# Kernel tuning notes

Hardware: AMD Instinct MI355X
Metric: run time of the kernel (lower is better)

Reference implementation:

```python
import jax, jax.numpy as jnp
import numpy as np
import math

D = 1024
H = 16
C = D // H
EPS = 1e-5

def layernorm(x, g, b):
    mu = jnp.mean(x, axis=-1, keepdims=True)
    var = jnp.mean(jnp.square(x - mu), axis=-1, keepdims=True)
    return (x - mu) * jax.lax.rsqrt(var + EPS) * g + b

def setup_inputs() -> dict:
    key = jax.random.key(0)
    ks = jax.random.split(key, 12)
    s = 1.0 / math.sqrt(D)
    inp = {
        "x": jax.random.normal(ks[0], (4, 2048, D), dtype=jnp.float32),
        "src_mask": jnp.ones((4, 2048), dtype=bool),
        "Wk": jax.random.normal(ks[1], (D, D), dtype=jnp.float32) * s,
        "Wq": jax.random.normal(ks[2], (D, D), dtype=jnp.float32) * s,
        "Wv": jax.random.normal(ks[3], (D, D), dtype=jnp.float32) * s,
        "Wfc": jax.random.normal(ks[4], (D, D), dtype=jnp.float32) * s,
        "bfc": jnp.zeros((D,), dtype=jnp.float32),
        "g1": jnp.ones((D,), dtype=jnp.float32),
        "b1": jnp.zeros((D,), dtype=jnp.float32),
        "g2": jnp.ones((D,), dtype=jnp.float32),
        "b2": jnp.zeros((D,), dtype=jnp.float32),
        "W1": jax.random.normal(ks[5], (D, 4 * D), dtype=jnp.float32) * s,
        "bf1": jnp.zeros((4 * D,), dtype=jnp.float32),
        "W2": jax.random.normal(ks[6], (4 * D, D), dtype=jnp.float32) * (1.0 / math.sqrt(4 * D)),
        "bf2": jnp.zeros((D,), dtype=jnp.float32),
    }
    return inp

def reference(x, src_mask, Wk, Wq, Wv, Wfc, bfc, g1, b1, g2, b2, W1, bf1, W2, bf2):
    b, s, _ = x.shape
    xl = layernorm(x, g1, b1)
    # self-attention (src_mask is unused in the original module)
    k = (xl @ Wk).reshape(b, s, H, C).transpose(0, 2, 1, 3)  # bhsc
    q = (xl @ Wq).reshape(b, s, H, C).transpose(0, 2, 1, 3)
    v = (xl @ Wv).reshape(b, s, H, C).transpose(0, 2, 1, 3)
    # NOTE: original multiplies by sqrt(c) (not divide) -- faithful quirk
    scores = jnp.einsum('bhqc,bhkc->bhqk', q, k) * math.sqrt(C)
    attn = jax.nn.softmax(scores, axis=-1)
    o = jnp.einsum('bhqk,bhkc->bhqc', attn, v)
    o = o.transpose(0, 2, 1, 3).reshape(b, s, D)
    ka = o @ Wfc + bfc
    x = ka + x
    xl2 = layernorm(x, g2, b2)
    ff = jax.nn.relu(xl2 @ W1 + bf1) @ W2 + bf2
    return ff + x
```

## Files before the change

### kernel.cpp

```cpp
#include <hip/hip_runtime.h>
#include <hip/hip_bf16.h>
#include <math.h>


typedef __hip_bfloat16 bf16_t;
typedef __bf16 bf16x8 __attribute__((ext_vector_type(8)));
typedef float f32x4 __attribute__((ext_vector_type(4)));

#define LN_EPS 1e-5f
#define QSCALE 11.541560327111707f
#define RESCALE_THR 100.0f
#define M0_PRIOR 275.0f

__device__ __forceinline__ void async_copy16(const bf16_t* g, bf16_t* l) {
  __builtin_amdgcn_global_load_lds(
      (const __attribute__((address_space(1))) void*)g,
      (__attribute__((address_space(3))) void*)l,
      16 , 0 , 0 );
}

__device__ __forceinline__ void split_bf16(float v, bf16_t& hi, bf16_t& lo) {
  hi = __float2bfloat16(v);
  lo = __float2bfloat16(v - __bfloat162float(hi));
}

template<bool SPLIT>
__global__ __launch_bounds__(256) void ln_kernel(
    const float* __restrict__ x, const float* __restrict__ g,
    const float* __restrict__ b, bf16_t* __restrict__ out_hi,
    bf16_t* __restrict__ out_lo)
{
  const int row = blockIdx.x;
  const int tid = threadIdx.x;
  const float4 v = *(const float4*)(x + (size_t)row * 1024 + tid * 4);
  float s  = v.x + v.y + v.z + v.w;
  float ss = v.x * v.x + v.y * v.y + v.z * v.z + v.w * v.w;
  for (int off = 32; off > 0; off >>= 1) {
    s  += __shfl_down(s, off);
    ss += __shfl_down(ss, off);
  }
  __shared__ float sb[4], ssb[4];
  const int wave = tid >> 6, lane = tid & 63;
  if (lane == 0) { sb[wave] = s; ssb[wave] = ss; }
  __syncthreads();
  const float tot  = sb[0] + sb[1] + sb[2] + sb[3];
  const float tots = ssb[0] + ssb[1] + ssb[2] + ssb[3];
  const float mu   = tot * (1.0f / 1024.0f);
  const float var  = tots * (1.0f / 1024.0f) - mu * mu;
  const float rstd = rsqrtf(var + LN_EPS);
  const float4 gv = *(const float4*)(g + tid * 4);
  const float4 bv = *(const float4*)(b + tid * 4);
  float y[4] = {(v.x - mu) * rstd * gv.x + bv.x,
                (v.y - mu) * rstd * gv.y + bv.y,
                (v.z - mu) * rstd * gv.z + bv.z,
                (v.w - mu) * rstd * gv.w + bv.w};
  bf16_t hi[4] __attribute__((aligned(8)));
  bf16_t lo[4] __attribute__((aligned(8)));
  #pragma unroll
  for (int i = 0; i < 4; i++) split_bf16(y[i], hi[i], lo[i]);
  uint2 ph, pl;
  __builtin_memcpy(&ph, hi, 8);
  *(uint2*)(out_hi + (size_t)row * 1024 + tid * 4) = ph;
  if (SPLIT) {
    __builtin_memcpy(&pl, lo, 8);
    *(uint2*)(out_lo + (size_t)row * 1024 + tid * 4) = pl;
  }
}

__global__ __launch_bounds__(256) void wtrans_all_kernel(
    const float* __restrict__ Wq, const float* __restrict__ Wk,
    const float* __restrict__ Wv, const float* __restrict__ Wfc,
    const float* __restrict__ W1, const float* __restrict__ W2,
    bf16_t* __restrict__ WqkH, bf16_t* __restrict__ WqkL,
    bf16_t* __restrict__ WvT, bf16_t* __restrict__ WfcT,
    bf16_t* __restrict__ W1T, bf16_t* __restrict__ W2T)
{
  const int id = blockIdx.x;
  const float* W; bf16_t* DH; bf16_t* DL = nullptr;
  int K, N, n0, k0;
  if (id < 4096) {
    K = 1024; N = 1024;
    const int local = id & 1023;
    n0 = (local & 31) * 32; k0 = (local >> 5) * 32;
    if (id < 1024)      { W = Wq;  DH = WqkH;                 DL = WqkL; }
    else if (id < 2048) { W = Wk;  DH = WqkH + 1024 * 1024;   DL = WqkL + 1024 * 1024; }
    else if (id < 3072) { W = Wv;  DH = WvT; }
    else                { W = Wfc; DH = WfcT; }
  } else if (id < 8192) {
    const int local = id - 4096;
    K = 1024; N = 4096; W = W1; DH = W1T;
    n0 = (local & 127) * 32; k0 = (local >> 7) * 32;
  } else {
    const int local = id - 8192;
    K = 4096; N = 1024; W = W2; DH = W2T;
    n0 = (local & 31) * 32; k0 = (local >> 5) * 32;
  }
  __shared__ float t[32][33];
  const int tx = threadIdx.x & 31, ty = threadIdx.x >> 5;
  #pragma unroll
  for (int r = ty; r < 32; r += 8)
    t[r][tx] = W[(size_t)(k0 + r) * N + n0 + tx];
  __syncthreads();
  #pragma unroll
  for (int r = ty; r < 32; r += 8) {
    const float v = t[tx][r];
    bf16_t hi, lo;
    split_bf16(v, hi, lo);
    DH[(size_t)(n0 + r) * K + k0 + tx] = hi;
    if (DL) DL[(size_t)(n0 + r) * K + k0 + tx] = lo;
  }
}

template<bool BIAS, bool RELU, bool RESID, bool OUTBF>
__global__ __launch_bounds__(256) void gemm_kernel(
    const bf16_t* __restrict__ A, const bf16_t* __restrict__ BT,
    const float* __restrict__ bias, const float* __restrict__ resid,
    float* __restrict__ outF, bf16_t* __restrict__ outB,
    int M, int N, int K)
{
  __shared__ __align__(16) bf16_t As[128 * 64];
  __shared__ __align__(16) bf16_t Bs[128 * 64];
  const int nblk = N >> 7;
  const int bm = blockIdx.x / nblk;
  const int bn = blockIdx.x % nblk;
  const int tid  = threadIdx.x;
  const int wave = tid >> 6;
  const int lane = tid & 63;
  const int l15  = lane & 15;
  const int quad = lane >> 4;
  const int wm = wave >> 1, wn = wave & 1;

  const int srow = lane >> 3;
  const int schunk = (lane & 7) ^ srow;
  const bf16_t* aG = A  + (size_t)(bm * 128 + wave * 32 + srow) * K + schunk * 8;
  const bf16_t* bG = BT + (size_t)(bn * 128 + wave * 32 + srow) * K + schunk * 8;

  f32x4 acc[4][4];
  #pragma unroll
  for (int i = 0; i < 4; i++)
    #pragma unroll
    for (int j = 0; j < 4; j++) acc[i][j] = (f32x4){0.f, 0.f, 0.f, 0.f};

  const int rsw = l15 & 7;

  for (int kt = 0; kt < K; kt += 64) {
    #pragma unroll
    for (int j = 0; j < 4; j++) {
      async_copy16(aG + kt + (size_t)(j * 8) * K, &As[(wave * 32 + j * 8) * 64]);
      async_copy16(bG + kt + (size_t)(j * 8) * K, &Bs[(wave * 32 + j * 8) * 64]);
    }
    __syncthreads();
    #pragma unroll
    for (int ko = 0; ko < 2; ko++) {
      bf16x8 af[4], bfr[4];
      #pragma unroll
      for (int i = 0; i < 4; i++)
        af[i]  = *(const bf16x8*)&As[(wm * 64 + i * 16 + l15) * 64 +
                                     (((ko * 4 + quad) ^ rsw) * 8)];
      #pragma unroll
      for (int j = 0; j < 4; j++)
        bfr[j] = *(const bf16x8*)&Bs[(wn * 64 + j * 16 + l15) * 64 +
                                     (((ko * 4 + quad) ^ rsw) * 8)];
      #pragma unroll
      for (int i = 0; i < 4; i++)
        #pragma unroll
        for (int j = 0; j < 4; j++)
          acc[i][j] = __builtin_amdgcn_mfma_f32_16x16x32_bf16(af[i], bfr[j], acc[i][j], 0, 0, 0);
    }
    __syncthreads();
  }

  const int gm0 = bm * 128 + wm * 64 + quad * 4;
  const int gn0 = bn * 128 + wn * 64 + l15;
  #pragma unroll
  for (int i = 0; i < 4; i++) {
    #pragma unroll
    for (int j = 0; j < 4; j++) {
      const int gn = gn0 + j * 16;
      const float bz = BIAS ? bias[gn] : 0.0f;
      #pragma unroll
      for (int r = 0; r < 4; r++) {
        const int gm = gm0 + i * 16 + r;
        float v = acc[i][j][r] + bz;
        if (RESID) v += resid[(size_t)gm * N + gn];
        if (RELU)  v = fmaxf(v, 0.0f);
        if (OUTBF) outB[(size_t)gm * N + gn] = __float2bfloat16(v);
        else       outF[(size_t)gm * N + gn] = v;
      }
    }
  }
}

__global__ __launch_bounds__(256) void gemm_split_kernel(
    const bf16_t* __restrict__ Ah, const bf16_t* __restrict__ Al,
    const bf16_t* __restrict__ Bh, const bf16_t* __restrict__ Bl,
    bf16_t* __restrict__ out_hi, bf16_t* __restrict__ out_lo,
    int M, int N, int K)
{
  __shared__ __align__(16) bf16_t AsH[128 * 32];
  __shared__ __align__(16) bf16_t AsL[128 * 32];
  __shared__ __align__(16) bf16_t BsH[128 * 32];
  __shared__ __align__(16) bf16_t BsL[128 * 32];
  const int nblk = N >> 7;
  const int bm = blockIdx.x / nblk;
  const int bn = blockIdx.x % nblk;
  const int tid  = threadIdx.x;
  const int wave = tid >> 6;
  const int lane = tid & 63;
  const int l15  = lane & 15;
  const int quad = lane >> 4;
  const int wm = wave >> 1, wn = wave & 1;

  const int srow = lane >> 2;
  const int schunk = (lane & 3) ^ ((lane >> 3) & 3);
  const size_t aOff = (size_t)(bm * 128 + wave * 32 + srow) * K + schunk * 8;
  const size_t bOff = (size_t)(bn * 128 + wave * 32 + srow) * K + schunk * 8;
  const int ldsOff0 = (wave * 32) * 32;
  const int ldsOff1 = (wave * 32 + 16) * 32;

  f32x4 acc[4][4];
  #pragma unroll
  for (int i = 0; i < 4; i++)
    #pragma unroll
    for (int j = 0; j < 4; j++) acc[i][j] = (f32x4){0.f, 0.f, 0.f, 0.f};

  const int rsw = (l15 >> 1) & 3;

  for (int kt = 0; kt < K; kt += 32) {
    async_copy16(Ah + aOff + kt, &AsH[ldsOff0]);
    async_copy16(Ah + aOff + kt + (size_t)16 * K, &AsH[ldsOff1]);
    async_copy16(Al + aOff + kt, &AsL[ldsOff0]);
    async_copy16(Al + aOff + kt + (size_t)16 * K, &AsL[ldsOff1]);
    async_copy16(Bh + bOff + kt, &BsH[ldsOff0]);
    async_copy16(Bh + bOff + kt + (size_t)16 * K, &BsH[ldsOff1]);
    async_copy16(Bl + bOff + kt, &BsL[ldsOff0]);
    async_copy16(Bl + bOff + kt + (size_t)16 * K, &BsL[ldsOff1]);
    __syncthreads();
    bf16x8 afH[4], afL[4], bfH[4], bfL[4];
    #pragma unroll
    for (int i = 0; i < 4; i++) {
      const int o = (wm * 64 + i * 16 + l15) * 32 + ((quad ^ rsw) * 8);
      afH[i] = *(const bf16x8*)&AsH[o];
      afL[i] = *(const bf16x8*)&AsL[o];
    }
    #pragma unroll
    for (int j = 0; j < 4; j++) {
      const int o = (wn * 64 + j * 16 + l15) * 32 + ((quad ^ rsw) * 8);
      bfH[j] = *(const bf16x8*)&BsH[o];
      bfL[j] = *(const bf16x8*)&BsL[o];
    }
    #pragma unroll
    for (int i = 0; i < 4; i++)
      #pragma unroll
      for (int j = 0; j < 4; j++) {
        acc[i][j] = __builtin_amdgcn_mfma_f32_16x16x32_bf16(afH[i], bfH[j], acc[i][j], 0, 0, 0);
        acc[i][j] = __builtin_amdgcn_mfma_f32_16x16x32_bf16(afH[i], bfL[j], acc[i][j], 0, 0, 0);
        acc[i][j] = __builtin_amdgcn_mfma_f32_16x16x32_bf16(afL[i], bfH[j], acc[i][j], 0, 0, 0);
      }
    __syncthreads();
  }

  const int gm0 = bm * 128 + wm * 64 + quad * 4;
  const int gn0 = bn * 128 + wn * 64 + l15;
  #pragma unroll
  for (int i = 0; i < 4; i++)
    #pragma unroll
    for (int j = 0; j < 4; j++) {
      const int gn = gn0 + j * 16;
      const float scale = (gn < 1024) ? QSCALE : 1.0f;
      #pragma unroll
      for (int r = 0; r < 4; r++) {
        const int gm = gm0 + i * 16 + r;
        bf16_t hi, lo;
        split_bf16(acc[i][j][r] * scale, hi, lo);
        out_hi[(size_t)gm * N + gn] = hi;
        out_lo[(size_t)gm * N + gn] = lo;
      }
    }
}

__global__ __launch_bounds__(256) void attn_kernel(
    const bf16_t* __restrict__ qkH,
    const bf16_t* __restrict__ qkL,
    const bf16_t* __restrict__ vT,
    bf16_t* __restrict__ o)
{
  const int lin   = blockIdx.x;
  const int slice = (lin & 7) * 8 + ((lin >> 3) & 7);
  const int qt    = lin >> 6;
  const int h     = slice & 15;
  const int b     = slice >> 4;
  const int wave = threadIdx.x >> 6;
  const int lane = threadIdx.x & 63;
  const int l15  = lane & 15;
  const int quad = lane >> 4;
  const int sw   = l15 & 7;
  const int qrowA = qt * 128 + wave * 32;
  const int qrowB = qrowA + 16;

  __shared__ __align__(16) bf16_t SMEM[20480];
  bf16_t* pw = SMEM + 16384 + wave * 1024;

  const size_t tok0 = (size_t)b * 2048;
  const size_t qoffA = (tok0 + qrowA + l15) * 2048 + h * 64;
  const size_t qoffB = (tok0 + qrowB + l15) * 2048 + h * 64;
  const bf16x8 aA0H = *(const bf16x8*)(qkH + qoffA + quad * 8);
  const bf16x8 aA1H = *(const bf16x8*)(qkH + qoffA + 32 + quad * 8);
  const bf16x8 aA0L = *(const bf16x8*)(qkL + qoffA + quad * 8);
  const bf16x8 aA1L = *(const bf16x8*)(qkL + qoffA + 32 + quad * 8);
  const bf16x8 aB0H = *(const bf16x8*)(qkH + qoffB + quad * 8);
  const bf16x8 aB1H = *(const bf16x8*)(qkH + qoffB + 32 + quad * 8);
  const bf16x8 aB0L = *(const bf16x8*)(qkL + qoffB + quad * 8);
  const bf16x8 aB1L = *(const bf16x8*)(qkL + qoffB + 32 + quad * 8);

  const int kOff = 1024 + h * 64;
  const int rsub = lane >> 3;
  const int csw  = (lane & 7) ^ rsub;

  const bf16_t* vRow[4];
  #pragma unroll
  for (int c = 0; c < 4; c++)
    vRow[c] = vT + (size_t)(h * 64 + c * 16 + l15) * 8192 + tok0 + quad * 8;

  f32x4 negMA = (f32x4){-M0_PRIOR, -M0_PRIOR, -M0_PRIOR, -M0_PRIOR};
  f32x4 negMB = negMA;
  f32x4 OfA[4], OfB[4];
  f32x4 lsumA = (f32x4){0.f, 0.f, 0.f, 0.f};
  f32x4 lsumB = lsumA;
  #pragma unroll
  for (int c = 0; c < 4; c++) { OfA[c] = lsumA; OfB[c] = lsumA; }

  #pragma unroll
  for (int j = 0; j < 2; j++) {
    const int row0 = wave * 16 + j * 8;
    const size_t krow = tok0 + row0 + rsub;
    async_copy16(qkH + krow * 2048 + kOff + csw * 8, &SMEM[row0 * 64]);
    async_copy16(qkL + krow * 2048 + kOff + csw * 8, &SMEM[8192 + row0 * 64]);
  }
  __syncthreads();

  for (int i = 0; i < 32; i++) {
    const int kbase = i * 64;
    const int co = (i & 1) * 4096;
    const int no = 4096 - co;
    if (i < 31) {
      #pragma unroll
      for (int j = 0; j < 2; j++) {
        const int row0 = wave * 16 + j * 8;
        const size_t krow = tok0 + kbase + 64 + row0 + rsub;
        async_copy16(qkH + krow * 2048 + kOff + csw * 8, &SMEM[no + row0 * 64]);
        async_copy16(qkL + krow * 2048 + kOff + csw * 8, &SMEM[8192 + no + row0 * 64]);
      }
    }
    const bf16_t* KhC = SMEM + co;
    const bf16_t* KlC = SMEM + 8192 + co;

    #pragma unroll
    for (int half = 0; half < 2; half++) {
      const int koff = kbase + half * 32;
      bf16x8 bv[4];
      #pragma unroll
      for (int c = 0; c < 4; c++)
        bv[c] = *(const bf16x8*)(vRow[c] + koff);

      #pragma unroll
      for (int tl = 0; tl < 2; tl++) {
        const int t = half * 2 + tl;
        const int base = (t * 16 + l15) * 64;
        const bf16x8 bh0 = *(const bf16x8*)&KhC[base + ((quad) ^ sw) * 8];
        const bf16x8 bh1 = *(const bf16x8*)&KhC[base + ((4 + quad) ^ sw) * 8];
        const bf16x8 bl0 = *(const bf16x8*)&KlC[base + ((quad) ^ sw) * 8];
        const bf16x8 bl1 = *(const bf16x8*)&KlC[base + ((4 + quad) ^ sw) * 8];
        f32x4 accA = negMA;
        f32x4 accB = negMB;
        __builtin_amdgcn_s_setprio(1);
        accA = __builtin_amdgcn_mfma_f32_16x16x32_bf16(aA0H, bh0, accA, 0, 0, 0);
        accA = __builtin_amdgcn_mfma_f32_16x16x32_bf16(aA1H, bh1, accA, 0, 0, 0);
        accA = __builtin_amdgcn_mfma_f32_16x16x32_bf16(aA0H, bl0, accA, 0, 0, 0);
        accA = __builtin_amdgcn_mfma_f32_16x16x32_bf16(aA1H, bl1, accA, 0, 0, 0);
        accA = __builtin_amdgcn_mfma_f32_16x16x32_bf16(aA0L, bh0, accA, 0, 0, 0);
        accA = __builtin_amdgcn_mfma_f32_16x16x32_bf16(aA1L, bh1, accA, 0, 0, 0);
        accB = __builtin_amdgcn_mfma_f32_16x16x32_bf16(aB0H, bh0, accB, 0, 0, 0);
        accB = __builtin_amdgcn_mfma_f32_16x16x32_bf16(aB1H, bh1, accB, 0, 0, 0);
        accB = __builtin_amdgcn_mfma_f32_16x16x32_bf16(aB0H, bl0, accB, 0, 0, 0);
        accB = __builtin_amdgcn_mfma_f32_16x16x32_bf16(aB1H, bl1, accB, 0, 0, 0);
        accB = __builtin_amdgcn_mfma_f32_16x16x32_bf16(aB0L, bh0, accB, 0, 0, 0);
        accB = __builtin_amdgcn_mfma_f32_16x16x32_bf16(aB1L, bh1, accB, 0, 0, 0);
        __builtin_amdgcn_s_setprio(0);

        float pmax = fmaxf(fmaxf(fmaxf(accA[0], accA[1]), fmaxf(accA[2], accA[3])),
                           fmaxf(fmaxf(accB[0], accB[1]), fmaxf(accB[2], accB[3])));
        if (!__all(pmax <= RESCALE_THR)) {
          #pragma unroll
          for (int r = 0; r < 4; r++) {
            float mA = accA[r], mB = accB[r];
            mA = fmaxf(mA, __shfl_xor(mA, 1)); mB = fmaxf(mB, __shfl_xor(mB, 1));
            mA = fmaxf(mA, __shfl_xor(mA, 2)); mB = fmaxf(mB, __shfl_xor(mB, 2));
            mA = fmaxf(mA, __shfl_xor(mA, 4)); mB = fmaxf(mB, __shfl_xor(mB, 4));
            mA = fmaxf(mA, __shfl_xor(mA, 8)); mB = fmaxf(mB, __shfl_xor(mB, 8));
            const float sA = fmaxf(mA, 0.0f);
            const float sB = fmaxf(mB, 0.0f);
            const float fA = __builtin_amdgcn_exp2f(-sA);
            const float fB = __builtin_amdgcn_exp2f(-sB);
            negMA[r] -= sA;  negMB[r] -= sB;
            lsumA[r] *= fA;  lsumB[r] *= fB;
            #pragma unroll
            for (int c = 0; c < 4; c++) { OfA[c][r] *= fA; OfB[c][r] *= fB; }
            accA[r] -= sA;   accB[r] -= sB;
            if (tl == 1) {
              const int RA = quad * 4 + r;
              const int RB = 16 + RA;
              const int ksw = (RA >> 1) & 3;
              const int iA = RA * 32 + (((l15 >> 3) ^ ksw) * 8) + (l15 & 7);
              const int iB = RB * 32 + (((l15 >> 3) ^ ksw) * 8) + (l15 & 7);
              pw[iA] = __float2bfloat16(__bfloat162float(pw[iA]) * fA);
              pw[iB] = __float2bfloat16(__bfloat162float(pw[iB]) * fB);
            }
          }
        }

        #pragma unroll
        for (int r = 0; r < 4; r++) {
          const float pA = __builtin_amdgcn_exp2f(accA[r]);
          const float pB = __builtin_amdgcn_exp2f(accB[r]);
          lsumA[r] += pA;
          lsumB[r] += pB;
          const int RA = quad * 4 + r;
          const int RB = 16 + RA;
          const int chunk = tl * 2 + (l15 >> 3);
          const int ksw = (RA >> 1) & 3;
          pw[RA * 32 + ((chunk ^ ksw) * 8) + (l15 & 7)] = __float2bfloat16(pA);
          pw[RB * 32 + ((chunk ^ ksw) * 8) + (l15 & 7)] = __float2bfloat16(pB);
        }
      }

      const int psw = (l15 >> 1) & 3;
      const bf16x8 paA = *(const bf16x8*)&pw[l15 * 32 + ((quad ^ psw) * 8)];
      const bf16x8 paB = *(const bf16x8*)&pw[(16 + l15) * 32 + ((quad ^ psw) * 8)];
      __builtin_amdgcn_s_setprio(1);
      #pragma unroll
      for (int c = 0; c < 4; c++) {
        OfA[c] = __builtin_amdgcn_mfma_f32_16x16x32_bf16(paA, bv[c], OfA[c], 0, 0, 0);
        OfB[c] = __builtin_amdgcn_mfma_f32_16x16x32_bf16(paB, bv[c], OfB[c], 0, 0, 0);
      }
      __builtin_amdgcn_s_setprio(0);
    }
    __syncthreads();
  }

  float lrowA[4], lrowB[4];
  #pragma unroll
  for (int r = 0; r < 4; r++) {
    float cA = lsumA[r], cB = lsumB[r];
    cA += __shfl_xor(cA, 1); cB += __shfl_xor(cB, 1);
    cA += __shfl_xor(cA, 2); cB += __shfl_xor(cB, 2);
    cA += __shfl_xor(cA, 4); cB += __shfl_xor(cB, 4);
    cA += __shfl_xor(cA, 8); cB += __shfl_xor(cB, 8);
    lrowA[r] = cA; lrowB[r] = cB;
  }

  bf16_t* opA = o + (tok0 + qrowA) * 1024 + h * 64;
  bf16_t* opB = o + (tok0 + qrowB) * 1024 + h * 64;
  #pragma unroll
  for (int c = 0; c < 4; c++)
    #pragma unroll
    for (int r = 0; r < 4; r++) {
      opA[(size_t)(quad * 4 + r) * 1024 + c * 16 + l15] =
          __float2bfloat16(OfA[c][r] / lrowA[r]);
      opB[(size_t)(quad * 4 + r) * 1024 + c * 16 + l15] =
          __float2bfloat16(OfB[c][r] / lrowB[r]);
    }
}

extern "C" void kernel_launch(void* const* d_in, const int* in_sizes, int n_in,
                              void* d_out, int out_size, void* d_ws, size_t ws_size,
                              hipStream_t stream)
{
  (void)in_sizes; (void)n_in; (void)out_size; (void)ws_size;
  const float* x   = (const float*)d_in[0];
  const float* Wk  = (const float*)d_in[2];
  const float* Wq  = (const float*)d_in[3];
  const float* Wv  = (const float*)d_in[4];
  const float* Wfc = (const float*)d_in[5];
  const float* bfc = (const float*)d_in[6];
  const float* g1  = (const float*)d_in[7];
  const float* b1  = (const float*)d_in[8];
  const float* g2  = (const float*)d_in[9];
  const float* b2  = (const float*)d_in[10];
  const float* W1  = (const float*)d_in[11];
  const float* bf1 = (const float*)d_in[12];
  const float* W2  = (const float*)d_in[13];
  const float* bf2 = (const float*)d_in[14];
  float* out = (float*)d_out;

  char* ws = (char*)d_ws;
  bf16_t* xl_hi  = (bf16_t*)(ws + (0ull   << 20));
  bf16_t* oAtt   = xl_hi;
  bf16_t* xl_lo  = (bf16_t*)(ws + (16ull  << 20));
  bf16_t* vT     = xl_lo;
  bf16_t* xl2    = xl_lo;
  bf16_t* qk_hi  = (bf16_t*)(ws + (32ull  << 20));
  bf16_t* qk_lo  = (bf16_t*)(ws + (64ull  << 20));
  bf16_t* h1     = qk_hi;
  float*  x2     = (float*) (ws + (112ull << 20));
  bf16_t* Wqk_hi = (bf16_t*)(ws + (144ull << 20));
  bf16_t* Wqk_lo = (bf16_t*)(ws + (148ull << 20));
  bf16_t* WvT    = (bf16_t*)(ws + (152ull << 20));
  bf16_t* WfcT   = (bf16_t*)(ws + (154ull << 20));
  bf16_t* W1T    = (bf16_t*)(ws + (156ull << 20));
  bf16_t* W2T    = (bf16_t*)(ws + (164ull << 20));

  const dim3 blk(256);

  wtrans_all_kernel<<<12288, blk, 0, stream>>>(
      Wq, Wk, Wv, Wfc, W1, W2, Wqk_hi, Wqk_lo, WvT, WfcT, W1T, W2T);

  ln_kernel<true><<<8192, blk, 0, stream>>>(x, g1, b1, xl_hi, xl_lo);

  gemm_split_kernel<<<64 * 16, blk, 0, stream>>>(
      xl_hi, xl_lo, Wqk_hi, Wqk_lo, qk_hi, qk_lo, 8192, 2048, 1024);

  gemm_kernel<false, false, false, true><<<8 * 64, blk, 0, stream>>>(
      WvT, xl_hi, nullptr, nullptr, nullptr, vT, 1024, 8192, 1024);

  attn_kernel<<<dim3(1024), blk, 0, stream>>>(qk_hi, qk_lo, vT, oAtt);

  gemm_kernel<true, false, true, false><<<64 * 8, blk, 0, stream>>>(
      oAtt, WfcT, bfc, x, x2, nullptr, 8192, 1024, 1024);

  ln_kernel<false><<<8192, blk, 0, stream>>>(x2, g2, b2, xl2, nullptr);

  gemm_kernel<true, true, false, true><<<64 * 32, blk, 0, stream>>>(
      xl2, W1T, bf1, nullptr, nullptr, h1, 8192, 4096, 1024);

  gemm_kernel<true, false, true, false><<<64 * 8, blk, 0, stream>>>(
      h1, W2T, bf2, x2, out, nullptr, 8192, 1024, 4096);
}
```

Measured before the change: 709.9 us.

## Transpose QK^T MFMA so softmax rows map to lanes; swizzle GEMM block order

The attention kernel swaps the MFMA operands for S=QK^T, so each lane holds four keys of one query row. Row max and row sum now use two cross-quad shuffles per tile instead of four per element, and P is written to LDS as packed 32-bit bf16 pairs. The rescale path and the final normalization fetch per-row factors with a lane shuffle and multiply by a reciprocal instead of dividing. Both GEMM kernels also remap block indices in groups of eight, aiming for better L2 locality across XCDs, at the cost of more intricate index logic.

```diff
diff --git a/kernel.cpp b/kernel.cpp
--- a/kernel.cpp
+++ b/kernel.cpp
@@ -22,6 +22,14 @@
 __device__ __forceinline__ void split_bf16(float v, bf16_t& hi, bf16_t& lo) {
   hi = __float2bfloat16(v);
   lo = __float2bfloat16(v - __bfloat162float(hi));
+}
+
+__device__ __forceinline__ unsigned pack_bf16(float lo, float hi) {
+  bf16_t a = __float2bfloat16(lo), b = __float2bfloat16(hi);
+  unsigned short ua, ub;
+  __builtin_memcpy(&ua, &a, 2);
+  __builtin_memcpy(&ub, &b, 2);
+  return (unsigned)ua | ((unsigned)ub << 16);
 }
 
 template<bool SPLIT>
@@ -121,8 +129,9 @@
   __shared__ __align__(16) bf16_t As[128 * 64];
   __shared__ __align__(16) bf16_t Bs[128 * 64];
   const int nblk = N >> 7;
-  const int bm = blockIdx.x / nblk;
-  const int bn = blockIdx.x % nblk;
+  const int wg = (blockIdx.x & 7) * (gridDim.x >> 3) + (blockIdx.x >> 3);
+  const int bm = wg / nblk;
+  const int bn = wg % nblk;
   const int tid  = threadIdx.x;
   const int wave = tid >> 6;
   const int lane = tid & 63;
@@ -202,8 +211,9 @@
   __shared__ __align__(16) bf16_t BsH[128 * 32];
   __shared__ __align__(16) bf16_t BsL[128 * 32];
   const int nblk = N >> 7;
-  const int bm = blockIdx.x / nblk;
-  const int bn = blockIdx.x % nblk;
+  const int wg = (blockIdx.x & 7) * (gridDim.x >> 3) + (blockIdx.x >> 3);
+  const int bm = wg / nblk;
+  const int bn = wg % nblk;
   const int tid  = threadIdx.x;
   const int wave = tid >> 6;
   const int lane = tid & 63;
@@ -300,6 +310,7 @@
 
   __shared__ __align__(16) bf16_t SMEM[20480];
   bf16_t* pw = SMEM + 16384 + wave * 1024;
+  unsigned* pw32 = (unsigned*)pw;
 
   const size_t tok0 = (size_t)b * 2048;
   const size_t qoffA = (tok0 + qrowA + l15) * 2048 + h * 64;
@@ -322,13 +333,18 @@
   for (int c = 0; c < 4; c++)
     vRow[c] = vT + (size_t)(h * 64 + c * 16 + l15) * 8192 + tok0 + quad * 8;
 
-  f32x4 negMA = (f32x4){-M0_PRIOR, -M0_PRIOR, -M0_PRIOR, -M0_PRIOR};
-  f32x4 negMB = negMA;
+  const int psw = (l15 >> 1) & 3;
+  const int wbaseA = l15 * 16 + (quad & 1) * 2;
+  const int wbaseB = wbaseA + 256;
+
+  float negMA = -M0_PRIOR, negMB = -M0_PRIOR;
+  float lsumA = 0.f, lsumB = 0.f;
   f32x4 OfA[4], OfB[4];
-  f32x4 lsumA = (f32x4){0.f, 0.f, 0.f, 0.f};
-  f32x4 lsumB = lsumA;
-  #pragma unroll
-  for (int c = 0; c < 4; c++) { OfA[c] = lsumA; OfB[c] = lsumA; }
+  #pragma unroll
+  for (int c = 0; c < 4; c++) {
+    OfA[c] = (f32x4){0.f, 0.f, 0.f, 0.f};
+    OfB[c] = (f32x4){0.f, 0.f, 0.f, 0.f};
+  }
 
   #pragma unroll
   for (int j = 0; j < 2; j++) {
@@ -371,70 +387,88 @@
         const bf16x8 bh1 = *(const bf16x8*)&KhC[base + ((4 + quad) ^ sw) * 8];
         const bf16x8 bl0 = *(const bf16x8*)&KlC[base + ((quad) ^ sw) * 8];
         const bf16x8 bl1 = *(const bf16x8*)&KlC[base + ((4 + quad) ^ sw) * 8];
-        f32x4 accA = negMA;
-        f32x4 accB = negMB;
+        f32x4 accA = (f32x4){negMA, negMA, negMA, negMA};
+        f32x4 accB = (f32x4){negMB, negMB, negMB, negMB};
         __builtin_amdgcn_s_setprio(1);
-        accA = __builtin_amdgcn_mfma_f32_16x16x32_bf16(aA0H, bh0, accA, 0, 0, 0);
-        accA = __builtin_amdgcn_mfma_f32_16x16x32_bf16(aA1H, bh1, accA, 0, 0, 0);
-        accA = __builtin_amdgcn_mfma_f32_16x16x32_bf16(aA0H, bl0, accA, 0, 0, 0);
-        accA = __builtin_amdgcn_mfma_f32_16x16x32_bf16(aA1H, bl1, accA, 0, 0, 0);
-        accA = __builtin_amdgcn_mfma_f32_16x16x32_bf16(aA0L, bh0, accA, 0, 0, 0);
-        accA = __builtin_amdgcn_mfma_f32_16x16x32_bf16(aA1L, bh1, accA, 0, 0, 0);
-        accB = __builtin_amdgcn_mfma_f32_16x16x32_bf16(aB0H, bh0, accB, 0, 0, 0);
-        accB = __builtin_amdgcn_mfma_f32_16x16x32_bf16(aB1H, bh1, accB, 0, 0, 0);
-        accB = __builtin_amdgcn_mfma_f32_16x16x32_bf16(aB0H, bl0, accB, 0, 0, 0);
-        accB = __builtin_amdgcn_mfma_f32_16x16x32_bf16(aB1H, bl1, accB, 0, 0, 0);
-        accB = __builtin_amdgcn_mfma_f32_16x16x32_bf16(aB0L, bh0, accB, 0, 0, 0);
-        accB = __builtin_amdgcn_mfma_f32_16x16x32_bf16(aB1L, bh1, accB, 0, 0, 0);
+        accA = __builtin_amdgcn_mfma_f32_16x16x32_bf16(bh0, aA0H, accA, 0, 0, 0);
+        accA = __builtin_amdgcn_mfma_f32_16x16x32_bf16(bh1, aA1H, accA, 0, 0, 0);
+        accA = __builtin_amdgcn_mfma_f32_16x16x32_bf16(bl0, aA0H, accA, 0, 0, 0);
+        accA = __builtin_amdgcn_mfma_f32_16x16x32_bf16(bl1, aA1H, accA, 0, 0, 0);
+        accA = __builtin_amdgcn_mfma_f32_16x16x32_bf16(bh0, aA0L, accA, 0, 0, 0);
+        accA = __builtin_amdgcn_mfma_f32_16x16x32_bf16(bh1, aA1L, accA, 0, 0, 0);
+        accB = __builtin_amdgcn_mfma_f32_16x16x32_bf16(bh0, aB0H, accB, 0, 0, 0);
+        accB = __builtin_amdgcn_mfma_f32_16x16x32_bf16(bh1, aB1H, accB, 0, 0, 0);
+        accB = __builtin_amdgcn_mfma_f32_16x16x32_bf16(bl0, aB0H, accB, 0, 0, 0);
+        accB = __builtin_amdgcn_mfma_f32_16x16x32_bf16(bl1, aB1H, accB, 0, 0, 0);
+        accB = __builtin_amdgcn_mfma_f32_16x16x32_bf16(bh0, aB0L, accB, 0, 0, 0);
+        accB = __builtin_amdgcn_mfma_f32_16x16x32_bf16(bh1, aB1L, accB, 0, 0, 0);
         __builtin_amdgcn_s_setprio(0);
 
         float pmax = fmaxf(fmaxf(fmaxf(accA[0], accA[1]), fmaxf(accA[2], accA[3])),
                            fmaxf(fmaxf(accB[0], accB[1]), fmaxf(accB[2], accB[3])));
         if (!__all(pmax <= RESCALE_THR)) {
+          float mA = fmaxf(fmaxf(accA[0], accA[1]), fmaxf(accA[2], accA[3]));
+          float mB = fmaxf(fmaxf(accB[0], accB[1]), fmaxf(accB[2], accB[3]));
+          mA = fmaxf(mA, __shfl_xor(mA, 16)); mB = fmaxf(mB, __shfl_xor(mB, 16));
+          mA = fmaxf(mA, __shfl_xor(mA, 32)); mB = fmaxf(mB, __shfl_xor(mB, 32));
+          const float sA = fmaxf(mA, 0.0f);
+          const float sB = fmaxf(mB, 0.0f);
+          const float fA = __builtin_amdgcn_exp2f(-sA);
+          const float fB = __builtin_amdgcn_exp2f(-sB);
+          negMA -= sA;  negMB -= sB;
+          lsumA *= fA;  lsumB *= fB;
           #pragma unroll
           for (int r = 0; r < 4; r++) {
-            float mA = accA[r], mB = accB[r];
-            mA = fmaxf(mA, __shfl_xor(mA, 1)); mB = fmaxf(mB, __shfl_xor(mB, 1));
-            mA = fmaxf(mA, __shfl_xor(mA, 2)); mB = fmaxf(mB, __shfl_xor(mB, 2));
-            mA = fmaxf(mA, __shfl_xor(mA, 4)); mB = fmaxf(mB, __shfl_xor(mB, 4));
-            mA = fmaxf(mA, __shfl_xor(mA, 8)); mB = fmaxf(mB, __shfl_xor(mB, 8));
-            const float sA = fmaxf(mA, 0.0f);
-            const float sB = fmaxf(mB, 0.0f);
-            const float fA = __builtin_amdgcn_exp2f(-sA);
-            const float fB = __builtin_amdgcn_exp2f(-sB);
-            negMA[r] -= sA;  negMB[r] -= sB;
-            lsumA[r] *= fA;  lsumB[r] *= fB;
+            accA[r] -= sA;  accB[r] -= sB;
+          }
+          #pragma unroll
+          for (int r = 0; r < 4; r++) {
+            const int src = quad * 20 + r;
+            const float fqA = __shfl(fA, src);
+            const float fqB = __shfl(fB, src);
             #pragma unroll
-            for (int c = 0; c < 4; c++) { OfA[c][r] *= fA; OfB[c][r] *= fB; }
-            accA[r] -= sA;   accB[r] -= sB;
-            if (tl == 1) {
-              const int RA = quad * 4 + r;
-              const int RB = 16 + RA;
-              const int ksw = (RA >> 1) & 3;
-              const int iA = RA * 32 + (((l15 >> 3) ^ ksw) * 8) + (l15 & 7);
-              const int iB = RB * 32 + (((l15 >> 3) ^ ksw) * 8) + (l15 & 7);
-              pw[iA] = __float2bfloat16(__bfloat162float(pw[iA]) * fA);
-              pw[iB] = __float2bfloat16(__bfloat162float(pw[iB]) * fB);
+            for (int c = 0; c < 4; c++) { OfA[c][r] *= fqA; OfB[c][r] *= fqB; }
+          }
+          if (tl == 1) {
+            asm volatile("" ::: "memory");
+            const int slot0 = (quad >> 1) ^ psw;
+            const int iA = wbaseA + slot0 * 4;
+            const int iB = wbaseB + slot0 * 4;
+            #pragma unroll
+            for (int j2 = 0; j2 < 2; j2++) {
+              unsigned ua = pw32[iA + j2], ub = pw32[iB + j2];
+              float a0 = __uint_as_float((ua & 0xffffu) << 16) * fA;
+              float a1 = __uint_as_float(ua & 0xffff0000u) * fA;
+              float b0 = __uint_as_float((ub & 0xffffu) << 16) * fB;
+              float b1 = __uint_as_float(ub & 0xffff0000u) * fB;
+              pw32[iA + j2] = pack_bf16(a0, a1);
+              pw32[iB + j2] = pack_bf16(b0, b1);
             }
+            asm volatile("" ::: "memory");
           }
         }
 
-        #pragma unroll
-        for (int r = 0; r < 4; r++) {
-          const float pA = __builtin_amdgcn_exp2f(accA[r]);
-          const float pB = __builtin_amdgcn_exp2f(accB[r]);
-          lsumA[r] += pA;
-          lsumB[r] += pB;
-          const int RA = quad * 4 + r;
-          const int RB = 16 + RA;
-          const int chunk = tl * 2 + (l15 >> 3);
-          const int ksw = (RA >> 1) & 3;
-          pw[RA * 32 + ((chunk ^ ksw) * 8) + (l15 & 7)] = __float2bfloat16(pA);
-          pw[RB * 32 + ((chunk ^ ksw) * 8) + (l15 & 7)] = __float2bfloat16(pB);
-        }
+        const float pA0 = __builtin_amdgcn_exp2f(accA[0]);
+        const float pA1 = __builtin_amdgcn_exp2f(accA[1]);
+        const float pA2 = __builtin_amdgcn_exp2f(accA[2]);
+        const float pA3 = __builtin_amdgcn_exp2f(accA[3]);
+        const float pB0 = __builtin_amdgcn_exp2f(accB[0]);
+        const float pB1 = __builtin_amdgcn_exp2f(accB[1]);
+        const float pB2 = __builtin_amdgcn_exp2f(accB[2]);
+        const float pB3 = __builtin_amdgcn_exp2f(accB[3]);
+        lsumA += (pA0 + pA1) + (pA2 + pA3);
+        lsumB += (pB0 + pB1) + (pB2 + pB3);
+        const int slot = ((tl * 2) + (quad >> 1)) ^ psw;
+        const int iA = wbaseA + slot * 4;
+        const int iB = wbaseB + slot * 4;
+        pw32[iA]     = pack_bf16(pA0, pA1);
+        pw32[iA + 1] = pack_bf16(pA2, pA3);
+        pw32[iB]     = pack_bf16(pB0, pB1);
+        pw32[iB + 1] = pack_bf16(pB2, pB3);
       }
 
-      const int psw = (l15 >> 1) & 3;
+      asm volatile("" ::: "memory");
+
       const bf16x8 paA = *(const bf16x8*)&pw[l15 * 32 + ((quad ^ psw) * 8)];
       const bf16x8 paB = *(const bf16x8*)&pw[(16 + l15) * 32 + ((quad ^ psw) * 8)];
       __builtin_amdgcn_s_setprio(1);
@@ -444,32 +478,31 @@
         OfB[c] = __builtin_amdgcn_mfma_f32_16x16x32_bf16(paB, bv[c], OfB[c], 0, 0, 0);
       }
       __builtin_amdgcn_s_setprio(0);
+
+      asm volatile("" ::: "memory");
     }
     __syncthreads();
   }
 
-  float lrowA[4], lrowB[4];
-  #pragma unroll
-  for (int r = 0; r < 4; r++) {
-    float cA = lsumA[r], cB = lsumB[r];
-    cA += __shfl_xor(cA, 1); cB += __shfl_xor(cB, 1);
-    cA += __shfl_xor(cA, 2); cB += __shfl_xor(cB, 2);
-    cA += __shfl_xor(cA, 4); cB += __shfl_xor(cB, 4);
-    cA += __shfl_xor(cA, 8); cB += __shfl_xor(cB, 8);
-    lrowA[r] = cA; lrowB[r] = cB;
-  }
+  float lrowA = lsumA, lrowB = lsumB;
+  lrowA += __shfl_xor(lrowA, 16); lrowB += __shfl_xor(lrowB, 16);
+  lrowA += __shfl_xor(lrowA, 32); lrowB += __shfl_xor(lrowB, 32);
 
   bf16_t* opA = o + (tok0 + qrowA) * 1024 + h * 64;
   bf16_t* opB = o + (tok0 + qrowB) * 1024 + h * 64;
   #pragma unroll
-  for (int c = 0; c < 4; c++)
-    #pragma unroll
-    for (int r = 0; r < 4; r++) {
+  for (int r = 0; r < 4; r++) {
+    const int src = quad * 20 + r;
+    const float rdA = 1.0f / __shfl(lrowA, src);
+    const float rdB = 1.0f / __shfl(lrowB, src);
+    #pragma unroll
+    for (int c = 0; c < 4; c++) {
       opA[(size_t)(quad * 4 + r) * 1024 + c * 16 + l15] =
-          __float2bfloat16(OfA[c][r] / lrowA[r]);
+          __float2bfloat16(OfA[c][r] * rdA);
       opB[(size_t)(quad * 4 + r) * 1024 + c * 16 + l15] =
-          __float2bfloat16(OfB[c][r] / lrowB[r]);
-    }
+          __float2bfloat16(OfB[c][r] * rdB);
+    }
+  }
 }
 
 extern "C" void kernel_launch(void* const* d_in, const int* in_sizes, int n_in,
```

Result: faster. 643.0 us, median of 2 (-9.4%).
